# Kernel tuning notes

Hardware: AMD Instinct MI355X
Metric: run time of the kernel (lower is better)

Reference implementation:

```python
import jax, jax.numpy as jnp
import numpy as np

B, L, D = 8, 512, 1024
NUM_SPANS = 6144  # L * max_width


def setup_inputs() -> dict:
    key = jax.random.key(0)
    k_h, k_s, k_w, k_b = jax.random.split(key, 4)
    h = jax.random.normal(k_h, (B, L, D), dtype=jnp.float32)
    span_idx = jax.random.randint(k_s, (B, NUM_SPANS, 2), 0, L, dtype=jnp.int64)
    # Linear(hidden, hidden) params (xavier-ish scale)
    lim = float(np.sqrt(6.0 / (D + D)))
    W = jax.random.uniform(k_w, (D, D), dtype=jnp.float32, minval=-lim, maxval=lim)
    b = jnp.zeros((D,), dtype=jnp.float32)
    return {"h": h, "span_idx": span_idx, "W": W, "b": b}


def reference(h, span_idx, W, b):
    # h: [B, L, D]; span_idx: [B, S, 2] with S = L * width
    Bb, Ll, Dd = h.shape
    start = jnp.clip(span_idx[..., 0], 0, Ll - 1)  # [B, S]
    end = jnp.clip(span_idx[..., 1], 0, Ll - 1)    # [B, S]
    valid = start <= end                            # [B, S]
    # prefix sums: cs[i, t] = sum_{u < t} h[i, u]  -> [B, L+1, D]
    cs = jnp.concatenate([jnp.zeros((Bb, 1, Dd), h.dtype), jnp.cumsum(h, axis=1)], axis=1)
    span_sum = (jnp.take_along_axis(cs, (end + 1)[:, :, None], axis=1)
                - jnp.take_along_axis(cs, start[:, :, None], axis=1))  # [B, S, D]
    count = (end - start + 1).astype(h.dtype)[:, :, None]
    span_rep = jnp.where(valid[:, :, None], span_sum / count, 0.0)  # [B, S, D]
    out = jax.nn.relu(jnp.einsum('bsd,ed->bse', span_rep, W) + b)
    return out.reshape(Bb, Ll, -1, Dd)
```

## Files before the change

### kernel.cpp

```cpp
#include <hip/hip_runtime.h>
#include <hip/hip_bf16.h>
#include <stdint.h>

#define B_DIM 8
#define L_DIM 512
#define D_DIM 1024
#define S_DIM 6144
#define NCHUNK 8
#define CHUNK (L_DIM / NCHUNK)
#define CSB (513 * 1024)

typedef __attribute__((ext_vector_type(8))) short short8;
typedef __attribute__((ext_vector_type(4))) float f32x4;
typedef __attribute__((ext_vector_type(8))) unsigned short us8;

__device__ __forceinline__ unsigned short bf16b(float x) {
    __hip_bfloat16 h = __float2bfloat16(x);
    return *reinterpret_cast<unsigned short*>(&h);
}

__device__ __forceinline__ unsigned short f2bf(float f) {
    unsigned int u = __float_as_uint(f);
    u += 0x7FFFu + ((u >> 16) & 1u);
    return (unsigned short)(u >> 16);
}

__global__ __launch_bounds__(256) void chunk_sums(const float* __restrict__ h,
                                                  float* __restrict__ csum) {
    int tid = blockIdx.x * 256 + threadIdx.x;
    int d = tid & 1023;
    int c = (tid >> 10) & 7;
    int b = tid >> 13;
    const float* hp = h + ((size_t)b * L_DIM + c * CHUNK) * D_DIM + d;
    float s = 0.f;
    #pragma unroll 8
    for (int i = 0; i < CHUNK; ++i) s += hp[(size_t)i * D_DIM];
    csum[tid] = s;
}

__global__ __launch_bounds__(256) void build_cs(const float* __restrict__ h,
                                                const float* __restrict__ csum,
                                                float* __restrict__ cs) {
    int tid = blockIdx.x * 256 + threadIdx.x;
    int d = tid & 1023;
    int c = (tid >> 10) & 7;
    int b = tid >> 13;
    float p = 0.f;
    for (int cc = 0; cc < c; ++cc)
        p += csum[(b << 13) + (cc << 10) + d];
    const float* hp = h + ((size_t)b * L_DIM + c * CHUNK) * D_DIM + d;
    float* cp = cs + ((size_t)b * (L_DIM + 1) + c * CHUNK) * D_DIM + d;
    if (c == 0) cp[0] = 0.f;
    #pragma unroll 8
    for (int i = 0; i < CHUNK; ++i) {
        p += hp[(size_t)i * D_DIM];
        cp[(size_t)(i + 1) * D_DIM] = p;
    }
}

__global__ __launch_bounds__(256) void wconv(const float* __restrict__ W,
                                             unsigned short* __restrict__ Wbf) {
    int tid = blockIdx.x * 256 + threadIdx.x;
    const float4* p = (const float4*)(W + (size_t)tid * 8);
    float4 a = p[0], c = p[1];
    us8 o;
    o[0] = f2bf(a.x); o[1] = f2bf(a.y); o[2] = f2bf(a.z); o[3] = f2bf(a.w);
    o[4] = f2bf(c.x); o[5] = f2bf(c.y); o[6] = f2bf(c.z); o[7] = f2bf(c.w);
    *(us8*)&Wbf[(size_t)tid * 8] = o;
}

__global__ __launch_bounds__(512, 4) void fused_gemm(
    const float* __restrict__ cs,
    const int* __restrict__ span_idx,
    const unsigned short* __restrict__ Wbf,
    const float* __restrict__ bias,
    float* __restrict__ out) {
    constexpr int K = D_DIM, N = D_DIM;
    __shared__ __align__(16) unsigned short As[128 * 64];
    __shared__ __align__(16) unsigned short Bs[2][256 * 64];

    const int tid = threadIdx.x;
    const int wid = tid >> 6, lane = tid & 63;
    const int widbase = wid << 6;

    int blk = blockIdx.x;
    int swz = (blk & 7) * 192 + (blk >> 3);
    const int bm = swz >> 2;
    const int bn = swz & 3;
    const int rowM = bm * 128;
    const int colN = bn * 256;
    const int b = bm / 48;
    const float* csb = cs + (size_t)b * CSB;

    const int ar0 = tid >> 3;
    const int ac8 = tid & 7;
    int2 se0 = ((const int2*)span_idx)[rowM + ar0];
    int2 se1 = ((const int2*)span_idx)[rowM + ar0 + 64];
    int st0 = min(max(se0.x, 0), L_DIM - 1), en0 = min(max(se0.y, 0), L_DIM - 1);
    int st1 = min(max(se1.x, 0), L_DIM - 1), en1 = min(max(se1.y, 0), L_DIM - 1);
    const float inv0 = (st0 <= en0) ? 1.0f / (float)(en0 - st0 + 1) : 0.0f;
    const float inv1 = (st1 <= en1) ? 1.0f / (float)(en1 - st1 + 1) : 0.0f;
    const float* pS0 = csb + (st0 << 10) + ac8 * 8;
    const float* pE0 = csb + ((en0 + 1) << 10) + ac8 * 8;
    const float* pS1 = csb + (st1 << 10) + ac8 * 8;
    const float* pE1 = csb + ((en1 + 1) << 10) + ac8 * 8;
    const int wa0 = ar0 * 128 + ((ac8 * 16) ^ ((ar0 & 7) << 4));
    const int wa1 = (ar0 + 64) * 128 + ((ac8 * 16) ^ ((ar0 & 7) << 4));

    const int fr = lane & 15;
    const int kq = lane >> 4;
    const int wr = wid >> 2, wc = wid & 3;

    f32x4 acc[4][4];
    #pragma unroll
    for (int i = 0; i < 4; ++i)
        #pragma unroll
        for (int j = 0; j < 4; ++j) acc[i][j] = (f32x4){0.f, 0.f, 0.f, 0.f};

    float4 eA0, eA1, sA0, sA1, eB0, eB1, sB0, sB1;

#define CS_LOAD(k0v) do { \
        eA0 = *(const float4*)(pE0 + (k0v));     eA1 = *(const float4*)(pE0 + (k0v) + 4); \
        sA0 = *(const float4*)(pS0 + (k0v));     sA1 = *(const float4*)(pS0 + (k0v) + 4); \
        eB0 = *(const float4*)(pE1 + (k0v));     eB1 = *(const float4*)(pE1 + (k0v) + 4); \
        sB0 = *(const float4*)(pS1 + (k0v));     sB1 = *(const float4*)(pS1 + (k0v) + 4); \
    } while (0)

#define A_WRITE() do { \
        us8 o0, o1; \
        o0[0] = bf16b((eA0.x - sA0.x) * inv0); o0[1] = bf16b((eA0.y - sA0.y) * inv0); \
        o0[2] = bf16b((eA0.z - sA0.z) * inv0); o0[3] = bf16b((eA0.w - sA0.w) * inv0); \
        o0[4] = bf16b((eA1.x - sA1.x) * inv0); o0[5] = bf16b((eA1.y - sA1.y) * inv0); \
        o0[6] = bf16b((eA1.z - sA1.z) * inv0); o0[7] = bf16b((eA1.w - sA1.w) * inv0); \
        o1[0] = bf16b((eB0.x - sB0.x) * inv1); o1[1] = bf16b((eB0.y - sB0.y) * inv1); \
        o1[2] = bf16b((eB0.z - sB0.z) * inv1); o1[3] = bf16b((eB0.w - sB0.w) * inv1); \
        o1[4] = bf16b((eB1.x - sB1.x) * inv1); o1[5] = bf16b((eB1.y - sB1.y) * inv1); \
        o1[6] = bf16b((eB1.z - sB1.z) * inv1); o1[7] = bf16b((eB1.w - sB1.w) * inv1); \
        *(us8*)((char*)As + wa0) = o0; \
        *(us8*)((char*)As + wa1) = o1; \
    } while (0)

#define STAGE_B(k0v, bufi) do { \
        _Pragma("unroll") \
        for (int i = 0; i < 4; ++i) { \
            int ci = i * 512 + tid; \
            int rB = ci >> 3, cB = ci & 7; \
            const unsigned short* srcB = Wbf + (size_t)(colN + rB) * K + (k0v) + ((cB ^ (rB & 7)) * 8); \
            __builtin_amdgcn_global_load_lds( \
                (const __attribute__((address_space(1))) void*)srcB, \
                (__attribute__((address_space(3))) void*)&Bs[bufi][(i * 512 + widbase) * 8], \
                16, 0, 0); \
        } \
    } while (0)

#define COMPUTE(bufi) do { \
        _Pragma("unroll") \
        for (int ks = 0; ks < 2; ++ks) { \
            const int kb = ks * 64 + kq * 16; \
            short8 af[4], bq[4]; \
            _Pragma("unroll") \
            for (int i = 0; i < 4; ++i) { \
                int ra = wr * 64 + i * 16 + fr; \
                af[i] = *(const short8*)((const char*)As + ra * 128 + (kb ^ ((ra & 7) << 4))); \
                int rb = wc * 64 + i * 16 + fr; \
                bq[i] = *(const short8*)((const char*)Bs[bufi] + rb * 128 + (kb ^ ((rb & 7) << 4))); \
            } \
            _Pragma("unroll") \
            for (int i = 0; i < 4; ++i) \
                _Pragma("unroll") \
                for (int j = 0; j < 4; ++j) \
                    acc[i][j] = __builtin_amdgcn_mfma_f32_16x16x32_bf16(af[i], bq[j], acc[i][j], 0, 0, 0); \
        } \
    } while (0)

    CS_LOAD(0);
    STAGE_B(0, 0);
    A_WRITE();
    __syncthreads();
    STAGE_B(64, 1);

    for (int t = 0; t < 16; ++t) {
        if (t < 15) CS_LOAD((t + 1) * 64);
        COMPUTE(t & 1);
        __syncthreads();
        if (t < 15) A_WRITE();
        __syncthreads();
        if (t < 14) STAGE_B((t + 2) * 64, t & 1);
    }

    const int m0 = rowM + wr * 64;
    const int n0 = colN + wc * 64;
    float bv[4];
    #pragma unroll
    for (int j = 0; j < 4; ++j) bv[j] = bias[n0 + j * 16 + fr];
    #pragma unroll
    for (int i = 0; i < 4; ++i)
        #pragma unroll
        for (int j = 0; j < 4; ++j)
            #pragma unroll
            for (int r = 0; r < 4; ++r) {
                int m = m0 + i * 16 + kq * 4 + r;
                int n = n0 + j * 16 + fr;
                float v = acc[i][j][r] + bv[j];
                out[(size_t)m * N + n] = v > 0.f ? v : 0.f;
            }
#undef CS_LOAD
#undef A_WRITE
#undef STAGE_B
#undef COMPUTE
}

extern "C" void kernel_launch(void* const* d_in, const int* in_sizes, int n_in,
                              void* d_out, int out_size, void* d_ws, size_t ws_size,
                              hipStream_t stream) {
    const float* h = (const float*)d_in[0];
    const int* span = (const int*)d_in[1];
    const float* W = (const float*)d_in[2];
    const float* bias = (const float*)d_in[3];
    float* out = (float*)d_out;

    char* ws = (char*)d_ws;
    float* cs = (float*)(ws);
    unsigned short* Wbf = (unsigned short*)(ws + 16809984);
    float* csum = (float*)(ws + 18907136);

    chunk_sums<<<256, 256, 0, stream>>>(h, csum);
    build_cs<<<256, 256, 0, stream>>>(h, csum, cs);
    wconv<<<512, 256, 0, stream>>>(W, Wbf);
    fused_gemm<<<1536, 512, 0, stream>>>(cs, span, Wbf, bias, out);
}
```

Measured before the change: 381.6 us.

## Double-buffer A tile and restructure GEMM pipeline with one barrier per step

Doubles the A shared-memory tile so the next A chunk can be converted and written while the current one is consumed. This lets each K-step use a single barrier with explicit vmcnt waits instead of two __syncthreads. Prefetch of cumulative-sum loads now runs two steps ahead, and MFMA sections are raised to high priority with s_setprio. LDS use grows and the launch-bounds occupancy hint drops from 4 to 2, which could reduce latency hiding. Correctness now depends on hand-counted waitcnt values.

Result: faster. 357.6 us (-6.3%).

```diff
diff --git a/kernel.cpp b/kernel.cpp
--- a/kernel.cpp
+++ b/kernel.cpp
@@ -69,14 +69,14 @@
     *(us8*)&Wbf[(size_t)tid * 8] = o;
 }
 
-__global__ __launch_bounds__(512, 4) void fused_gemm(
+__global__ __launch_bounds__(512, 2) void fused_gemm(
     const float* __restrict__ cs,
     const int* __restrict__ span_idx,
     const unsigned short* __restrict__ Wbf,
     const float* __restrict__ bias,
     float* __restrict__ out) {
     constexpr int K = D_DIM, N = D_DIM;
-    __shared__ __align__(16) unsigned short As[128 * 64];
+    __shared__ __align__(16) unsigned short As[2][128 * 64];
     __shared__ __align__(16) unsigned short Bs[2][256 * 64];
 
     const int tid = threadIdx.x;
@@ -119,14 +119,17 @@
 
     float4 eA0, eA1, sA0, sA1, eB0, eB1, sB0, sB1;
 
-#define CS_LOAD(k0v) do { \
+#define FENCE() do { asm volatile("" ::: "memory"); \
+                     __builtin_amdgcn_sched_barrier(0); } while (0)
+
+#define CS_ISSUE(k0v) do { \
         eA0 = *(const float4*)(pE0 + (k0v));     eA1 = *(const float4*)(pE0 + (k0v) + 4); \
         sA0 = *(const float4*)(pS0 + (k0v));     sA1 = *(const float4*)(pS0 + (k0v) + 4); \
         eB0 = *(const float4*)(pE1 + (k0v));     eB1 = *(const float4*)(pE1 + (k0v) + 4); \
         sB0 = *(const float4*)(pS1 + (k0v));     sB1 = *(const float4*)(pS1 + (k0v) + 4); \
     } while (0)
 
-#define A_WRITE() do { \
+#define A_CONV_WRITE(bufi) do { \
         us8 o0, o1; \
         o0[0] = bf16b((eA0.x - sA0.x) * inv0); o0[1] = bf16b((eA0.y - sA0.y) * inv0); \
         o0[2] = bf16b((eA0.z - sA0.z) * inv0); o0[3] = bf16b((eA0.w - sA0.w) * inv0); \
@@ -136,8 +139,8 @@
         o1[2] = bf16b((eB0.z - sB0.z) * inv1); o1[3] = bf16b((eB0.w - sB0.w) * inv1); \
         o1[4] = bf16b((eB1.x - sB1.x) * inv1); o1[5] = bf16b((eB1.y - sB1.y) * inv1); \
         o1[6] = bf16b((eB1.z - sB1.z) * inv1); o1[7] = bf16b((eB1.w - sB1.w) * inv1); \
-        *(us8*)((char*)As + wa0) = o0; \
-        *(us8*)((char*)As + wa1) = o1; \
+        *(us8*)((char*)As[bufi] + wa0) = o0; \
+        *(us8*)((char*)As[bufi] + wa1) = o1; \
     } while (0)
 
 #define STAGE_B(k0v, bufi) do { \
@@ -161,31 +164,51 @@
             _Pragma("unroll") \
             for (int i = 0; i < 4; ++i) { \
                 int ra = wr * 64 + i * 16 + fr; \
-                af[i] = *(const short8*)((const char*)As + ra * 128 + (kb ^ ((ra & 7) << 4))); \
+                af[i] = *(const short8*)((const char*)As[bufi] + ra * 128 + (kb ^ ((ra & 7) << 4))); \
                 int rb = wc * 64 + i * 16 + fr; \
                 bq[i] = *(const short8*)((const char*)Bs[bufi] + rb * 128 + (kb ^ ((rb & 7) << 4))); \
             } \
+            __builtin_amdgcn_s_setprio(1); \
             _Pragma("unroll") \
             for (int i = 0; i < 4; ++i) \
                 _Pragma("unroll") \
                 for (int j = 0; j < 4; ++j) \
                     acc[i][j] = __builtin_amdgcn_mfma_f32_16x16x32_bf16(af[i], bq[j], acc[i][j], 0, 0, 0); \
+            __builtin_amdgcn_s_setprio(0); \
         } \
     } while (0)
 
-    CS_LOAD(0);
+    CS_ISSUE(0);
+    FENCE();
     STAGE_B(0, 0);
-    A_WRITE();
-    __syncthreads();
+    FENCE();
+    A_CONV_WRITE(0);
+    CS_ISSUE(64);
+    FENCE();
+    asm volatile("s_waitcnt vmcnt(8) lgkmcnt(0)" ::: "memory");
+    __builtin_amdgcn_s_barrier();
+    FENCE();
     STAGE_B(64, 1);
+    FENCE();
 
     for (int t = 0; t < 16; ++t) {
-        if (t < 15) CS_LOAD((t + 1) * 64);
-        COMPUTE(t & 1);
-        __syncthreads();
-        if (t < 15) A_WRITE();
-        __syncthreads();
-        if (t < 14) STAGE_B((t + 2) * 64, t & 1);
+        const int cur = t & 1;
+        COMPUTE(cur);
+        if (t < 15) {
+            A_CONV_WRITE(cur ^ 1);
+            if (t < 14) CS_ISSUE((t + 2) * 64);
+            FENCE();
+            if (t < 14)
+                asm volatile("s_waitcnt vmcnt(8) lgkmcnt(0)" ::: "memory");
+            else
+                asm volatile("s_waitcnt vmcnt(0) lgkmcnt(0)" ::: "memory");
+            __builtin_amdgcn_s_barrier();
+            FENCE();
+            if (t < 14) {
+                STAGE_B((t + 2) * 64, cur);
+                FENCE();
+            }
+        }
     }
 
     const int m0 = rowM + wr * 64;
@@ -204,8 +227,9 @@
                 float v = acc[i][j][r] + bv[j];
                 out[(size_t)m * N + n] = v > 0.f ? v : 0.f;
             }
-#undef CS_LOAD
-#undef A_WRITE
+#undef FENCE
+#undef CS_ISSUE
+#undef A_CONV_WRITE
 #undef STAGE_B
 #undef COMPUTE
 }
```
